# Optimization experiments

Hardware: AMD Instinct MI355X
Metric: run time of the kernel (lower is better)

## Reference

```python
import jax, jax.numpy as jnp
import numpy as np
from jax.scipy.special import logsumexp

HIDDEN = 512
KEY_DIM = HIDDEN // 8  # 64
B, N, M = 4, 2048, 2048
EPS_IN = 1e-5  # InstanceNorm2d default eps
N_ITERS = 20


def setup_inputs() -> dict:
    key = jax.random.key(0)
    k = jax.random.split(key, 6)
    bound = 1.0 / np.sqrt(HIDDEN)  # nn.Linear default init range
    return {
        "x": jax.random.normal(k[0], (B, N, HIDDEN), dtype=jnp.float32),
        "y": jax.random.normal(k[1], (B, M, HIDDEN), dtype=jnp.float32),
        "Wq": jax.random.uniform(k[2], (KEY_DIM, HIDDEN), jnp.float32, -bound, bound),
        "bq": jax.random.uniform(k[3], (KEY_DIM,), jnp.float32, -bound, bound),
        "in_w": jnp.ones((1,), jnp.float32),   # InstanceNorm2d affine weight
        "in_b": jnp.zeros((1,), jnp.float32),  # InstanceNorm2d affine bias
    }


def _sinkhorn_slack(log_alpha, n_iters):
    # log_alpha: [B, J, K]; pad with a zero slack row and column -> [B, J+1, K+1]
    la = jnp.pad(log_alpha, ((0, 0), (0, 1), (0, 1)))

    def step(la, _):
        top = la[:, :-1, :]
        top = top - logsumexp(top, axis=2, keepdims=True)
        la = jnp.concatenate([top, la[:, -1:, :]], axis=1)
        left = la[:, :, :-1]
        left = left - logsumexp(left, axis=1, keepdims=True)
        la = jnp.concatenate([left, la[:, :, -1:]], axis=2)
        return la, None

    la, _ = jax.lax.scan(step, la, None, length=n_iters)
    return la[:, :-1, :-1]


def reference(x, y, Wq, bq, in_w, in_b):
    # linear projection to key_dim
    xw = jnp.einsum('bnh,kh->bnk', x, Wq) + bq  # [B,N,K]
    yw = jnp.einsum('bmh,kh->bmk', y, Wq) + bq  # [B,M,K]
    # pairwise squared euclidean distance [B,N,M]
    dist = (jnp.sum(xw * xw, axis=-1)[:, :, None]
            + jnp.sum(yw * yw, axis=-1)[:, None, :]
            - 2.0 * jnp.einsum('bnk,bmk->bnm', xw, yw))
    e = jnp.exp(-dist)
    # InstanceNorm2d(1, affine=True): normalize each [N,M] map per batch element
    mean = jnp.mean(e, axis=(1, 2), keepdims=True)
    var = jnp.mean((e - mean) ** 2, axis=(1, 2), keepdims=True)
    dist_s = (e - mean) / jnp.sqrt(var + EPS_IN) * in_w[0] + in_b[0]
    # 20-iter slack Sinkhorn in log space
    log_ds = _sinkhorn_slack(dist_s, N_ITERS)
    ds = jnp.exp(log_ds)
    atweight = jnp.max(ds, axis=-1, keepdims=True)  # [B,N,1]
    attention = jnp.einsum('bni,bmi->bnm', atweight, atweight)  # [B,N,N]
    return attention
```

## Files before the change

kernel.cpp:

```cpp
#include <hip/hip_runtime.h>
#include <hip/hip_bf16.h>

constexpr int B = 4, N = 2048, M = 2048, H = 512, ITERS = 20;
constexpr float EPS_IN = 1e-5f;
constexpr float LOG2E = 1.4426950408889634f;
constexpr float LN2 = 0.6931471805599453f;

typedef unsigned short ushort_t;
typedef unsigned int uint_t;
typedef __attribute__((ext_vector_type(8))) short bf16x8;
typedef __attribute__((ext_vector_type(4))) float f32x4;

__device__ __forceinline__ float fexp2(float x) { return __builtin_amdgcn_exp2f(x); }
__device__ __forceinline__ float flog2(float x) { return __builtin_amdgcn_logf(x); }
__device__ __forceinline__ float blo(uint_t v) { return __uint_as_float(v << 16); }
__device__ __forceinline__ float bhi(uint_t v) { return __uint_as_float(v & 0xffff0000u); }
__device__ __forceinline__ uint_t bf16rn(float f) {
  uint_t x = __float_as_uint(f);
  return (x + 0x7fffu + ((x >> 16) & 1u)) >> 16;
}

__global__ __launch_bounds__(256) void wqconv_kernel(
    const float* __restrict__ Wq, ushort_t* __restrict__ wqh) {
  int g = blockIdx.x * 256 + threadIdx.x;
  float4 v = *(const float4*)(Wq + (size_t)g * 4);
  uint2 pk;
  pk.x = bf16rn(v.x) | (bf16rn(v.y) << 16);
  pk.y = bf16rn(v.z) | (bf16rn(v.w) << 16);
  *(uint2*)(wqh + (size_t)g * 4) = pk;
}

__global__ __launch_bounds__(256) void proj_kernel(
    const float* __restrict__ x, const float* __restrict__ y,
    const ushort_t* __restrict__ wqh, const float* __restrict__ bq,
    ushort_t* __restrict__ qwf, float* __restrict__ norms,
    float* __restrict__ stats) {
  int t = threadIdx.x;
  if (blockIdx.x == 0 && t < 32) stats[t] = 0.0f;
  int w = t >> 6, lane = t & 63;
  int fr = lane & 15, fh = (lane >> 4) * 8;
  int rw = blockIdx.x * 64 + w * 16;
  int row = rw + fr;
  const float* src = (row < B * N) ? x + (size_t)row * H
                                   : y + (size_t)(row - B * N) * H;

  f32x4 acc[4];
#pragma unroll
  for (int j = 0; j < 4; j++) acc[j] = (f32x4){0.f, 0.f, 0.f, 0.f};

#pragma unroll
  for (int ks = 0; ks < 16; ks++) {
    float4 a0 = *(const float4*)(src + ks * 32 + fh);
    float4 a1 = *(const float4*)(src + ks * 32 + fh + 4);
    union { uint4 u; bf16x8 h; } ac;
    ac.u.x = bf16rn(a0.x) | (bf16rn(a0.y) << 16);
    ac.u.y = bf16rn(a0.z) | (bf16rn(a0.w) << 16);
    ac.u.z = bf16rn(a1.x) | (bf16rn(a1.y) << 16);
    ac.u.w = bf16rn(a1.z) | (bf16rn(a1.w) << 16);
    bf16x8 aF = ac.h;
#pragma unroll
    for (int j = 0; j < 4; j++) {
      bf16x8 bF = *(const bf16x8*)(wqh + (size_t)(j * 16 + fr) * H + ks * 32 + fh);
      acc[j] = __builtin_amdgcn_mfma_f32_16x16x32_bf16(aF, bF, acc[j], 0, 0, 0);
    }
  }

  float bqv[4];
#pragma unroll
  for (int j = 0; j < 4; j++) bqv[j] = bq[j * 16 + fr];

  size_t gbase = (size_t)(rw >> 4) * 1024;
#pragma unroll
  for (int reg = 0; reg < 4; reg++) {
    int rr = ((lane >> 4) << 2) + reg;
    int r = rw + rr;
    float nr = 0.0f;
#pragma unroll
    for (int j = 0; j < 4; j++) {
      float vv = acc[j][reg] + bqv[j];
      qwf[gbase + (size_t)(j * 2 + (fr >> 3)) * 128 + rr * 8 + (fr & 7)] =
          (ushort_t)bf16rn(vv);
      nr = fmaf(vv, vv, nr);
    }
    nr += __shfl_xor(nr, 1, 64);
    nr += __shfl_xor(nr, 2, 64);
    nr += __shfl_xor(nr, 4, 64);
    nr += __shfl_xor(nr, 8, 64);
    if (fr == 0) norms[r] = nr;
  }
}

__global__ __launch_bounds__(256) void dist_kernel(
    const ushort_t* __restrict__ qwf, const float* __restrict__ norms,
    ushort_t* __restrict__ e, float* __restrict__ stats) {
  __shared__ __align__(16) ushort_t eT[128 * 136];
  __shared__ float xnL[128], ynL[128], scr[12];
  int t = threadIdx.x;
  int b = blockIdx.z;
  int n0 = blockIdx.x * 128, m0 = blockIdx.y * 128;
  int w = t >> 6, lane = t & 63;

  if (t < 128) xnL[t] = norms[b * N + n0 + t];
  else ynL[t - 128] = norms[B * N + b * M + m0 + (t - 128)];

  int wr = (w >> 1) * 64, wc = (w & 1) * 64;

  f32x4 acc[4][4];
#pragma unroll
  for (int i = 0; i < 4; i++)
#pragma unroll
    for (int j = 0; j < 4; j++) acc[i][j] = (f32x4){0.f, 0.f, 0.f, 0.f};

  const ushort_t* xg = qwf + (size_t)((b * N + n0 + wr) >> 4) * 1024 + lane * 8;
  const ushort_t* yg = qwf + (size_t)((B * N + b * M + m0 + wc) >> 4) * 1024 + lane * 8;
#pragma unroll
  for (int kg = 0; kg < 2; kg++) {
    bf16x8 aF[4], bF[4];
#pragma unroll
    for (int i = 0; i < 4; i++) {
      aF[i] = *(const bf16x8*)(xg + (size_t)i * 1024 + kg * 512);
      bF[i] = *(const bf16x8*)(yg + (size_t)i * 1024 + kg * 512);
    }
#pragma unroll
    for (int i = 0; i < 4; i++)
#pragma unroll
      for (int j = 0; j < 4; j++)
        acc[i][j] = __builtin_amdgcn_mfma_f32_16x16x32_bf16(
            aF[i], bF[j], acc[i][j], 0, 0, 0);
  }
  __syncthreads();

  float lsum = 0.0f, lsq = 0.0f, lmax = 0.0f;
#pragma unroll
  for (int i = 0; i < 4; i++) {
    int rl = wr + i * 16 + ((lane >> 4) << 2);
    float xn0 = xnL[rl], xn1 = xnL[rl + 1], xn2 = xnL[rl + 2], xn3 = xnL[rl + 3];
#pragma unroll
    for (int j = 0; j < 4; j++) {
      int cl = wc + j * 16 + (lane & 15);
      float yn_ = ynL[cl];
      float v0 = __expf(-(xn0 + yn_ - 2.0f * acc[i][j][0]));
      float v1 = __expf(-(xn1 + yn_ - 2.0f * acc[i][j][1]));
      float v2 = __expf(-(xn2 + yn_ - 2.0f * acc[i][j][2]));
      float v3 = __expf(-(xn3 + yn_ - 2.0f * acc[i][j][3]));
      lsum += (v0 + v1) + (v2 + v3);
      lsq += (v0 * v0 + v1 * v1) + (v2 * v2 + v3 * v3);
      lmax = fmaxf(fmaxf(lmax, fmaxf(v0, v1)), fmaxf(v2, v3));
      eT[(rl + 0) * 136 + cl] = (ushort_t)bf16rn(v0);
      eT[(rl + 1) * 136 + cl] = (ushort_t)bf16rn(v1);
      eT[(rl + 2) * 136 + cl] = (ushort_t)bf16rn(v2);
      eT[(rl + 3) * 136 + cl] = (ushort_t)bf16rn(v3);
    }
  }
#pragma unroll
  for (int off = 32; off; off >>= 1) {
    lsum += __shfl_xor(lsum, off, 64);
    lsq += __shfl_xor(lsq, off, 64);
    lmax = fmaxf(lmax, __shfl_xor(lmax, off, 64));
  }
  if (lane == 0) { scr[w] = lsum; scr[4 + w] = lsq; scr[8 + w] = lmax; }
  __syncthreads();

#pragma unroll
  for (int p = 0; p < 8; p++) {
    int row = p * 16 + (t >> 4);
    int cs = (t & 15) * 8;
    uint4 vv = *(const uint4*)&eT[row * 136 + cs];
    *(uint4*)(e + (size_t)(b * N + n0 + row) * M + m0 + cs) = vv;
  }
  if (t == 0) {
    float ssum = scr[0] + scr[1] + scr[2] + scr[3];
    float ssq = scr[4] + scr[5] + scr[6] + scr[7];
    float smax = fmaxf(fmaxf(scr[8], scr[9]), fmaxf(scr[10], scr[11]));
    atomicAdd(&stats[b * 4 + 0], ssum);
    atomicAdd(&stats[b * 4 + 1], ssq);
    atomicMax((unsigned int*)&stats[b * 4 + 2], __float_as_uint(smax));
  }
}

__global__ void params_csinit_kernel(const float* __restrict__ stats,
                                     const float* __restrict__ in_w,
                                     const float* __restrict__ in_b,
                                     float* __restrict__ params,
                                     float* __restrict__ csb) {
  int g = blockIdx.x * 256 + threadIdx.x;
  *(float4*)(csb + g * 4) = float4{0.f, 0.f, 0.f, 0.f};
  if (blockIdx.x == 0 && threadIdx.x < B) {
    int b = threadIdx.x;
    float NMf = (float)N * (float)M;
    float mean = stats[b * 4 + 0] / NMf;
    float var = stats[b * 4 + 1] / NMf - mean * mean;
    var = fmaxf(var, 0.0f);
    float stdv = sqrtf(var + EPS_IN);
    float s = in_w[0] / stdv;
    float t = in_b[0] - mean * s;
    float emax = __uint_as_float(((const unsigned int*)stats)[b * 4 + 2]);
    float Amax = fmaxf(fmaf(s, emax, t), t);
    float KK = fmaxf(Amax - 60.0f, 0.0f);
    params[b * 8 + 0] = s * LOG2E;
    params[b * 8 + 1] = (t - 2.0f * KK) * LOG2E;
    params[b * 8 + 2] = KK;
    params[b * 8 + 3] = __expf(-KK);
    params[b * 8 + 4] = __expf(KK);
  }
}

#define PASS1(uu, off, PA, PB)                           \
  {                                                      \
    float4 ca = *(const float4*)&C2a[(off) + ln4];       \
    float4 cb = *(const float4*)&C2b[(off) + ln4];       \
    PA.x = fexp2(fmaf(blo(uu.x), sL, ca.x));             \
    PA.y = fexp2(fmaf(bhi(uu.x), sL, ca.y));             \
    PA.z = fexp2(fmaf(blo(uu.y), sL, ca.z));             \
    PA.w = fexp2(fmaf(bhi(uu.y), sL, ca.w));             \
    PB.x = fexp2(fmaf(blo(uu.z), sL, cb.x));             \
    PB.y = fexp2(fmaf(bhi(uu.z), sL, cb.y));             \
    PB.z = fexp2(fmaf(blo(uu.w), sL, cb.z));             \
    PB.w = fexp2(fmaf(bhi(uu.w), sL, cb.w));             \
    s0 += PA.x + PB.x;                                   \
    s1 += PA.y + PB.y;                                   \
    s2 += PA.z + PB.z;                                   \
    s3 += PA.w + PB.w;                                   \
  }

#define PASS2(PA, PB, AA, BB)                            \
  {                                                      \
    AA.x = fmaf(PA.x, g, AA.x);                          \
    AA.y = fmaf(PA.y, g, AA.y);                          \
    AA.z = fmaf(PA.z, g, AA.z);                          \
    AA.w = fmaf(PA.w, g, AA.w);                          \
    BB.x = fmaf(PB.x, g, BB.x);                          \
    BB.y = fmaf(PB.y, g, BB.y);                          \
    BB.z = fmaf(PB.z, g, BB.z);                          \
    BB.w = fmaf(PB.w, g, BB.w);                          \
  }

#define DO_ROW(q0, q1, q2, q3, ridx)                                   \
  {                                                                    \
    float s0 = 0, s1 = 0, s2 = 0, s3 = 0;                              \
    PASS1(q0, 0, pA0, pB0)                                             \
    PASS1(q1, 256, pA1, pB1)                                           \
    PASS1(q2, 512, pA2, pB2)                                           \
    PASS1(q3, 768, pA3, pB3)                                           \
    float sum = (s0 + s1) + (s2 + s3);                                 \
    _Pragma("unroll")                                                  \
    for (int off = 32; off; off >>= 1) sum += __shfl_xor(sum, off, 64);\
    float sumtot = sum + enk;                                          \
    float ls = flog2(sumtot);                                          \
    if (lane == 0) R[b * N + (ridx)] = KK + LN2 * ls;                  \
    float g = fexp2(-KK * LOG2E - ls);                                 \
    PASS2(pA0, pB0, accA0, accB0)                                      \
    PASS2(pA1, pB1, accA1, accB1)                                      \
    PASS2(pA2, pB2, accA2, accB2)                                      \
    PASS2(pA3, pB3, accA3, accB3)                                      \
  }

#define COMBINE8(cA, cB)                                               \
  {                                                                    \
    float4 q;                                                          \
    q = *(float4*)&cA[ln4];                                            \
    q.x += accA0.x; q.y += accA0.y; q.z += accA0.z; q.w += accA0.w;    \
    *(float4*)&cA[ln4] = q;                                            \
    q = *(float4*)&cA[256 + ln4];                                      \
    q.x += accA1.x; q.y += accA1.y; q.z += accA1.z; q.w += accA1.w;    \
    *(float4*)&cA[256 + ln4] = q;                                      \
    q = *(float4*)&cA[512 + ln4];                                      \
    q.x += accA2.x; q.y += accA2.y; q.z += accA2.z; q.w += accA2.w;    \
    *(float4*)&cA[512 + ln4] = q;                                      \
    q = *(float4*)&cA[768 + ln4];                                      \
    q.x += accA3.x; q.y += accA3.y; q.z += accA3.z; q.w += accA3.w;    \
    *(float4*)&cA[768 + ln4] = q;                                      \
    q = *(float4*)&cB[ln4];                                            \
    q.x += accB0.x; q.y += accB0.y; q.z += accB0.z; q.w += accB0.w;    \
    *(float4*)&cB[ln4] = q;                                            \
    q = *(float4*)&cB[256 + ln4];                                      \
    q.x += accB1.x; q.y += accB1.y; q.z += accB1.z; q.w += accB1.w;    \
    *(float4*)&cB[256 + ln4] = q;                                      \
    q = *(float4*)&cB[512 + ln4];                                      \
    q.x += accB2.x; q.y += accB2.y; q.z += accB2.z; q.w += accB2.w;    \
    *(float4*)&cB[512 + ln4] = q;                                      \
    q = *(float4*)&cB[768 + ln4];                                      \
    q.x += accB3.x; q.y += accB3.y; q.z += accB3.z; q.w += accB3.w;    \
    *(float4*)&cB[768 + ln4] = q;                                      \
  }

#define STORE8(cA, cB)                                                 \
  {                                                                    \
    *(float4*)&cA[ln4] = accA0;                                        \
    *(float4*)&cA[256 + ln4] = accA1;                                  \
    *(float4*)&cA[512 + ln4] = accA2;                                  \
    *(float4*)&cA[768 + ln4] = accA3;                                  \
    *(float4*)&cB[ln4] = accB0;                                        \
    *(float4*)&cB[256 + ln4] = accB1;                                  \
    *(float4*)&cB[512 + ln4] = accB2;                                  \
    *(float4*)&cB[768 + ln4] = accB3;                                  \
  }

__global__ __launch_bounds__(512) void sink_pass(
    const ushort_t* __restrict__ e, const float* __restrict__ params,
    const float* __restrict__ cs_cur, float* __restrict__ cs_nxt,
    float* __restrict__ cs_zz, float* __restrict__ R) {
  __shared__ __align__(16) float C2a[1024], C2b[1024];
  __shared__ __align__(16) float Ds[2048];
  __shared__ __align__(16) float colA[1024], colB[1024];
  __shared__ __align__(16) float colA2[1024], colB2[1024];
  int t = threadIdx.x;
  int b = blockIdx.y, blk = blockIdx.x;
  int w = t >> 6, lane = t & 63;
  int ln4 = lane * 4;
  const float* pr = params + b * 8;
  float sL = pr[0], c0L = pr[1], KK = pr[2], enk = pr[3], ekk = pr[4];

  int r0 = blk * 32 + w * 4;
  const ushort_t* ep = e + (size_t)(b * N + r0) * M + lane * 8;
  uint4 u0 = *(const uint4*)(ep);
  uint4 u1 = *(const uint4*)(ep + 512);
  uint4 u2 = *(const uint4*)(ep + 1024);
  uint4 u3 = *(const uint4*)(ep + 1536);
  const ushort_t* ep2 = ep + M;
  uint4 v0 = *(const uint4*)(ep2);
  uint4 v1 = *(const uint4*)(ep2 + 512);
  uint4 v2 = *(const uint4*)(ep2 + 1024);
  uint4 v3 = *(const uint4*)(ep2 + 1536);

  if (blk == 0) {
    *(float4*)(cs_zz + b * M + t * 4) = float4{0.f, 0.f, 0.f, 0.f};
  }
  if (t < 256) {
    float4 c0 = *(const float4*)(cs_cur + b * M + t * 8);
    float4 c1 = *(const float4*)(cs_cur + b * M + t * 8 + 4);
    c0.x += enk; c0.y += enk; c0.z += enk; c0.w += enk;
    c1.x += enk; c1.y += enk; c1.z += enk; c1.w += enk;
    float4 ca, cb;
    ca.x = c0L - flog2(c0.x); ca.y = c0L - flog2(c0.y);
    ca.z = c0L - flog2(c0.z); ca.w = c0L - flog2(c0.w);
    cb.x = c0L - flog2(c1.x); cb.y = c0L - flog2(c1.y);
    cb.z = c0L - flog2(c1.z); cb.w = c0L - flog2(c1.w);
    *(float4*)&C2a[w * 256 + ln4] = ca;
    *(float4*)&C2b[w * 256 + ln4] = cb;
    float4 d0 = {ekk * c0.x, ekk * c0.y, ekk * c0.z, ekk * c0.w};
    float4 d1 = {ekk * c1.x, ekk * c1.y, ekk * c1.z, ekk * c1.w};
    *(float4*)&Ds[t * 8] = d0;
    *(float4*)&Ds[t * 8 + 4] = d1;
  }
  __syncthreads();

  float4 accA0 = {0,0,0,0}, accA1 = {0,0,0,0}, accA2 = {0,0,0,0}, accA3 = {0,0,0,0};
  float4 accB0 = {0,0,0,0}, accB1 = {0,0,0,0}, accB2 = {0,0,0,0}, accB3 = {0,0,0,0};
  float4 pA0, pA1, pA2, pA3, pB0, pB1, pB2, pB3;

  DO_ROW(u0, u1, u2, u3, r0)
  {
    const ushort_t* ep3 = ep + 2 * M;
    u0 = *(const uint4*)(ep3);
    u1 = *(const uint4*)(ep3 + 512);
    u2 = *(const uint4*)(ep3 + 1024);
    u3 = *(const uint4*)(ep3 + 1536);
  }
  DO_ROW(v0, v1, v2, v3, r0 + 1)
  {
    const ushort_t* ep4 = ep + 3 * M;
    v0 = *(const uint4*)(ep4);
    v1 = *(const uint4*)(ep4 + 512);
    v2 = *(const uint4*)(ep4 + 1024);
    v3 = *(const uint4*)(ep4 + 1536);
  }
  DO_ROW(u0, u1, u2, u3, r0 + 2)
  DO_ROW(v0, v1, v2, v3, r0 + 3)

  for (int ww = 0; ww < 4; ww++) {
    if (w == ww) {
      if (ww == 0) STORE8(colA, colB) else COMBINE8(colA, colB)
    } else if (w == ww + 4) {
      if (ww == 0) STORE8(colA2, colB2) else COMBINE8(colA2, colB2)
    }
    __syncthreads();
  }
  {
    int q = t & 7;
    const float* s1 = (q < 4) ? colA : colB;
    const float* s2 = (q < 4) ? colA2 : colB2;
    int qq = q & 3;
#pragma unroll
    for (int k = 0; k < 4; k++) {
      int j = k * 512 + t;
      int idx = (j >> 9) * 256 + ((j >> 3) & 63) * 4 + qq;
      atomicAdd(&cs_nxt[b * M + j], (s1[idx] + s2[idx]) * Ds[j]);
    }
  }
}

__global__ __launch_bounds__(256) void awmax_kernel(
    const ushort_t* __restrict__ e, const float* __restrict__ params,
    const float* __restrict__ cs_fin, const float* __restrict__ R,
    float* __restrict__ aw) {
  __shared__ __align__(16) float C2a[1024], C2b[1024];
  int t = threadIdx.x;
  int b = blockIdx.y, blk = blockIdx.x;
  const float* pr = params + b * 8;
  float sL = pr[0], c0L = pr[1], KK = pr[2], enk = pr[3];
  {
    float4 v0 = *(const float4*)(cs_fin + b * M + t * 8);
    float4 v1 = *(const float4*)(cs_fin + b * M + t * 8 + 4);
    float4 ca, cb;
    ca.x = c0L - flog2(v0.x + enk); ca.y = c0L - flog2(v0.y + enk);
    ca.z = c0L - flog2(v0.z + enk); ca.w = c0L - flog2(v0.w + enk);
    cb.x = c0L - flog2(v1.x + enk); cb.y = c0L - flog2(v1.y + enk);
    cb.z = c0L - flog2(v1.z + enk); cb.w = c0L - flog2(v1.w + enk);
    int it = t >> 6, ln = t & 63;
    *(float4*)&C2a[it * 256 + ln * 4] = ca;
    *(float4*)&C2b[it * 256 + ln * 4] = cb;
  }
  __syncthreads();

  int w = t >> 6, lane = t & 63;
  int ln4 = lane * 4;
  int r0 = blk * 16 + w * 4;
  const ushort_t* erow = e + (size_t)(b * N + r0) * M;
#pragma unroll
  for (int rr = 0; rr < 4; rr++) {
    float mx = -3.4e38f;
#pragma unroll
    for (int it = 0; it < 4; it++) {
      uint4 u = *(const uint4*)(erow + (size_t)rr * M + it * 512 + lane * 8);
      float4 ca = *(const float4*)&C2a[it * 256 + ln4];
      float4 cb = *(const float4*)&C2b[it * 256 + ln4];
      mx = fmaxf(mx, fmaf(blo(u.x), sL, ca.x));
      mx = fmaxf(mx, fmaf(bhi(u.x), sL, ca.y));
      mx = fmaxf(mx, fmaf(blo(u.y), sL, ca.z));
      mx = fmaxf(mx, fmaf(bhi(u.y), sL, ca.w));
      mx = fmaxf(mx, fmaf(blo(u.z), sL, cb.x));
      mx = fmaxf(mx, fmaf(bhi(u.z), sL, cb.y));
      mx = fmaxf(mx, fmaf(blo(u.w), sL, cb.z));
      mx = fmaxf(mx, fmaf(bhi(u.w), sL, cb.w));
    }
#pragma unroll
    for (int off = 32; off; off >>= 1) mx = fmaxf(mx, __shfl_xor(mx, off, 64));
    if (lane == 0) {
      float Rr = R[b * N + r0 + rr];
      aw[b * N + r0 + rr] = fexp2(mx + (KK - Rr) * LOG2E);
    }
  }
}

__global__ __launch_bounds__(256) void outer_kernel(const float* __restrict__ aw,
                                                    float* __restrict__ out) {
  size_t idx = (size_t)blockIdx.x * 256 + threadIdx.x;
  int b = (int)(idx >> 20);
  size_t rem = idx & ((1u << 20) - 1);
  int n = (int)(rem >> 9);
  int m4 = (int)(rem & 511) << 2;
  float a = aw[b * N + n];
  float4 wv = *(const float4*)(aw + b * N + m4);
  float4 o = {a * wv.x, a * wv.y, a * wv.z, a * wv.w};
  *(float4*)(out + (idx << 2)) = o;
}

extern "C" void kernel_launch(void* const* d_in, const int* in_sizes, int n_in,
                              void* d_out, int out_size, void* d_ws, size_t ws_size,
                              hipStream_t stream) {
  const float* x = (const float*)d_in[0];
  const float* y = (const float*)d_in[1];
  const float* Wq = (const float*)d_in[2];
  const float* bq = (const float*)d_in[3];
  const float* in_w = (const float*)d_in[4];
  const float* in_b = (const float*)d_in[5];
  ushort_t* e = (ushort_t*)d_out;

  float* ws = (float*)d_ws;
  ushort_t* qwf = (ushort_t*)ws;
  float* norms = ws + 1048576;
  float* R = norms + 16384;
  float* csb0 = R + 8192;
  float* csb1 = csb0 + 8192;
  float* csb2 = csb1 + 8192;
  float* aw = csb2 + 8192;
  float* stats = aw + 8192;
  float* params = stats + 32;
  ushort_t* wqh = (ushort_t*)(params + 32);
  float* csb[3] = {csb0, csb1, csb2};

  wqconv_kernel<<<32, 256, 0, stream>>>(Wq, wqh);
  proj_kernel<<<256, 256, 0, stream>>>(x, y, wqh, bq, qwf, norms, stats);
  dist_kernel<<<dim3(16, 16, B), 256, 0, stream>>>(qwf, norms, e, stats);
  params_csinit_kernel<<<24, 256, 0, stream>>>(stats, in_w, in_b, params, csb0);

  for (int it = 0; it < ITERS; it++) {
    sink_pass<<<dim3(64, B), 512, 0, stream>>>(
        e, params, csb[it % 3], csb[(it + 1) % 3], csb[(it + 2) % 3], R);
  }
  awmax_kernel<<<dim3(128, B), 256, 0, stream>>>(e, params, csb[ITERS % 3], R, aw);
  outer_kernel<<<16384, 256, 0, stream>>>(aw, (float*)d_out);
}
```

Baseline: 266.1 us.

## Store dist tile directly via swapped MFMA and split column-sum atomics into four copies

The dist kernel swaps the MFMA operands so each lane holds four consecutive columns of one row. It then writes packed bf16 pairs straight to global memory, dropping the LDS transpose buffer and one barrier. The Sinkhorn column-sum accumulators are replicated four times, indexed by block id, to cut atomic contention on each address. Consumers then sum the four copies on read, which costs extra loads and zeroing plus a larger workspace.

Result: slower. 273.8 us (+2.9%).

```diff
diff --git a/kernel.cpp b/kernel.cpp
--- a/kernel.cpp
+++ b/kernel.cpp
@@ -93,7 +93,6 @@
 __global__ __launch_bounds__(256) void dist_kernel(
     const ushort_t* __restrict__ qwf, const float* __restrict__ norms,
     ushort_t* __restrict__ e, float* __restrict__ stats) {
-  __shared__ __align__(16) ushort_t eT[128 * 136];
   __shared__ float xnL[128], ynL[128], scr[12];
   int t = threadIdx.x;
   int b = blockIdx.z;
@@ -126,30 +125,31 @@
 #pragma unroll
       for (int j = 0; j < 4; j++)
         acc[i][j] = __builtin_amdgcn_mfma_f32_16x16x32_bf16(
-            aF[i], bF[j], acc[i][j], 0, 0, 0);
+            bF[j], aF[i], acc[i][j], 0, 0, 0);
   }
   __syncthreads();
 
   float lsum = 0.0f, lsq = 0.0f, lmax = 0.0f;
 #pragma unroll
   for (int i = 0; i < 4; i++) {
-    int rl = wr + i * 16 + ((lane >> 4) << 2);
-    float xn0 = xnL[rl], xn1 = xnL[rl + 1], xn2 = xnL[rl + 2], xn3 = xnL[rl + 3];
+    int nl = wr + i * 16 + (lane & 15);
+    float xn_ = xnL[nl];
+    const size_t rowbase = (size_t)(b * N + n0 + nl) * M + m0;
 #pragma unroll
     for (int j = 0; j < 4; j++) {
-      int cl = wc + j * 16 + (lane & 15);
-      float yn_ = ynL[cl];
-      float v0 = __expf(-(xn0 + yn_ - 2.0f * acc[i][j][0]));
-      float v1 = __expf(-(xn1 + yn_ - 2.0f * acc[i][j][1]));
-      float v2 = __expf(-(xn2 + yn_ - 2.0f * acc[i][j][2]));
-      float v3 = __expf(-(xn3 + yn_ - 2.0f * acc[i][j][3]));
+      int mb = wc + j * 16 + ((lane >> 4) << 2);
+      float4 yn4 = *(const float4*)&ynL[mb];
+      float v0 = __expf(-(xn_ + yn4.x - 2.0f * acc[i][j][0]));
+      float v1 = __expf(-(xn_ + yn4.y - 2.0f * acc[i][j][1]));
+      float v2 = __expf(-(xn_ + yn4.z - 2.0f * acc[i][j][2]));
+      float v3 = __expf(-(xn_ + yn4.w - 2.0f * acc[i][j][3]));
       lsum += (v0 + v1) + (v2 + v3);
       lsq += (v0 * v0 + v1 * v1) + (v2 * v2 + v3 * v3);
       lmax = fmaxf(fmaxf(lmax, fmaxf(v0, v1)), fmaxf(v2, v3));
-      eT[(rl + 0) * 136 + cl] = (ushort_t)bf16rn(v0);
-      eT[(rl + 1) * 136 + cl] = (ushort_t)bf16rn(v1);
-      eT[(rl + 2) * 136 + cl] = (ushort_t)bf16rn(v2);
-      eT[(rl + 3) * 136 + cl] = (ushort_t)bf16rn(v3);
+      uint2 pk;
+      pk.x = bf16rn(v0) | (bf16rn(v1) << 16);
+      pk.y = bf16rn(v2) | (bf16rn(v3) << 16);
+      *(uint2*)(e + rowbase + mb) = pk;
     }
   }
 #pragma unroll
@@ -160,14 +160,6 @@
   }
   if (lane == 0) { scr[w] = lsum; scr[4 + w] = lsq; scr[8 + w] = lmax; }
   __syncthreads();
-
-#pragma unroll
-  for (int p = 0; p < 8; p++) {
-    int row = p * 16 + (t >> 4);
-    int cs = (t & 15) * 8;
-    uint4 vv = *(const uint4*)&eT[row * 136 + cs];
-    *(uint4*)(e + (size_t)(b * N + n0 + row) * M + m0 + cs) = vv;
-  }
   if (t == 0) {
     float ssum = scr[0] + scr[1] + scr[2] + scr[3];
     float ssq = scr[4] + scr[5] + scr[6] + scr[7];
@@ -324,11 +316,21 @@
   uint4 v3 = *(const uint4*)(ep2 + 1536);
 
   if (blk == 0) {
-    *(float4*)(cs_zz + b * M + t * 4) = float4{0.f, 0.f, 0.f, 0.f};
+#pragma unroll
+    for (int c = 0; c < 4; c++)
+      *(float4*)(cs_zz + c * 8192 + b * M + t * 4) = float4{0.f, 0.f, 0.f, 0.f};
   }
   if (t < 256) {
-    float4 c0 = *(const float4*)(cs_cur + b * M + t * 8);
-    float4 c1 = *(const float4*)(cs_cur + b * M + t * 8 + 4);
+    const float* cb0 = cs_cur + b * M + t * 8;
+    float4 c0 = *(const float4*)(cb0);
+    float4 c1 = *(const float4*)(cb0 + 4);
+#pragma unroll
+    for (int c = 1; c < 4; c++) {
+      float4 d0 = *(const float4*)(cb0 + c * 8192);
+      float4 d1 = *(const float4*)(cb0 + c * 8192 + 4);
+      c0.x += d0.x; c0.y += d0.y; c0.z += d0.z; c0.w += d0.w;
+      c1.x += d1.x; c1.y += d1.y; c1.z += d1.z; c1.w += d1.w;
+    }
     c0.x += enk; c0.y += enk; c0.z += enk; c0.w += enk;
     c1.x += enk; c1.y += enk; c1.z += enk; c1.w += enk;
     float4 ca, cb;
@@ -381,11 +383,12 @@
     const float* s1 = (q < 4) ? colA : colB;
     const float* s2 = (q < 4) ? colA2 : colB2;
     int qq = q & 3;
+    float* dst = cs_nxt + (blk & 3) * 8192 + b * M;
 #pragma unroll
     for (int k = 0; k < 4; k++) {
       int j = k * 512 + t;
       int idx = (j >> 9) * 256 + ((j >> 3) & 63) * 4 + qq;
-      atomicAdd(&cs_nxt[b * M + j], (s1[idx] + s2[idx]) * Ds[j]);
+      atomicAdd(&dst[j], (s1[idx] + s2[idx]) * Ds[j]);
     }
   }
 }
@@ -400,8 +403,16 @@
   const float* pr = params + b * 8;
   float sL = pr[0], c0L = pr[1], KK = pr[2], enk = pr[3];
   {
-    float4 v0 = *(const float4*)(cs_fin + b * M + t * 8);
-    float4 v1 = *(const float4*)(cs_fin + b * M + t * 8 + 4);
+    const float* cb0 = cs_fin + b * M + t * 8;
+    float4 v0 = *(const float4*)(cb0);
+    float4 v1 = *(const float4*)(cb0 + 4);
+#pragma unroll
+    for (int c = 1; c < 4; c++) {
+      float4 d0 = *(const float4*)(cb0 + c * 8192);
+      float4 d1 = *(const float4*)(cb0 + c * 8192 + 4);
+      v0.x += d0.x; v0.y += d0.y; v0.z += d0.z; v0.w += d0.w;
+      v1.x += d1.x; v1.y += d1.y; v1.z += d1.z; v1.w += d1.w;
+    }
     float4 ca, cb;
     ca.x = c0L - flog2(v0.x + enk); ca.y = c0L - flog2(v0.y + enk);
     ca.z = c0L - flog2(v0.z + enk); ca.w = c0L - flog2(v0.w + enk);
@@ -471,24 +482,24 @@
   ushort_t* qwf = (ushort_t*)ws;
   float* norms = ws + 1048576;
   float* R = norms + 16384;
-  float* csb0 = R + 8192;
-  float* csb1 = csb0 + 8192;
-  float* csb2 = csb1 + 8192;
-  float* aw = csb2 + 8192;
+  float* csb = R + 8192;
+  float* aw = csb + 98304;
   float* stats = aw + 8192;
   float* params = stats + 32;
   ushort_t* wqh = (ushort_t*)(params + 32);
-  float* csb[3] = {csb0, csb1, csb2};
 
   wqconv_kernel<<<32, 256, 0, stream>>>(Wq, wqh);
   proj_kernel<<<256, 256, 0, stream>>>(x, y, wqh, bq, qwf, norms, stats);
   dist_kernel<<<dim3(16, 16, B), 256, 0, stream>>>(qwf, norms, e, stats);
-  params_csinit_kernel<<<24, 256, 0, stream>>>(stats, in_w, in_b, params, csb0);
+  params_csinit_kernel<<<96, 256, 0, stream>>>(stats, in_w, in_b, params, csb);
 
   for (int it = 0; it < ITERS; it++) {
-    sink_pass<<<dim3(64, B), 512, 0, stream>>>(
-        e, params, csb[it % 3], csb[(it + 1) % 3], csb[(it + 2) % 3], R);
-  }
-  awmax_kernel<<<dim3(128, B), 256, 0, stream>>>(e, params, csb[ITERS % 3], R, aw);
+    float* cur = csb + (size_t)(it % 3) * 32768;
+    float* nxt = csb + (size_t)((it + 1) % 3) * 32768;
+    float* zz = csb + (size_t)((it + 2) % 3) * 32768;
+    sink_pass<<<dim3(64, B), 512, 0, stream>>>(e, params, cur, nxt, zz, R);
+  }
+  awmax_kernel<<<dim3(128, B), 256, 0, stream>>>(
+      e, params, csb + (size_t)(ITERS % 3) * 32768, R, aw);
   outer_kernel<<<16384, 256, 0, stream>>>(aw, (float*)d_out);
 }
```
